# Kernel tuning notes

Measured on AMD Instinct MI355X. Metric: run time of the kernel, lower is better.

## Reference

```python
import jax, jax.numpy as jnp
import numpy as np

B, M, C, D, FF, FEAT = 1, 1024, 128, 512, 1024, 20
PAIR = 3 * D + 2 * FEAT  # slow_scorer_size = 1576


def _ffnn(x, W0, b0, W1, b1):
    # FFNN(depth=1): hidden relu layer then linear output (eval mode, no dropout)
    return jax.nn.relu(x @ W0 + b0) @ W1 + b1


def _batch_gather(x, idx):
    # x: [B, M, ...], idx: [B, ...] int -> gather along mention dim per batch
    return jax.vmap(lambda xb, ib: xb[ib])(x, idx)


def _bucket_distance(d):
    # log-scale distance buckets 0..9 (identity for d<=4)
    log_idx = jnp.floor(jnp.log(jnp.maximum(d, 1).astype(jnp.float32)) / jnp.log(2.0)).astype(jnp.int32) + 3
    return jnp.clip(jnp.where(d <= 4, d, log_idx), 0, 9)


def setup_inputs() -> dict:
    key = jax.random.key(0)
    ks = jax.random.split(key, 10)
    s = 0.02
    return {
        'mention_emb': jax.random.normal(ks[0], (B, M, D), dtype=jnp.float32),
        'mention_cluster_ids': jax.random.randint(ks[1], (B, M), 0, 200),
        'mention_speaker_ids': jax.random.randint(ks[2], (B, M), 0, 2),
        'ms_W0': jax.random.normal(ks[3], (D, FF), dtype=jnp.float32) * s,
        'ms_b0': jnp.zeros((FF,), jnp.float32),
        'ms_W1': jax.random.normal(ks[4], (FF, 1), dtype=jnp.float32) * s,
        'ms_b1': jnp.zeros((1,), jnp.float32),
        'sp_W0': jax.random.normal(ks[5], (PAIR, FF), dtype=jnp.float32) * s,
        'sp_b0': jnp.zeros((FF,), jnp.float32),
        'sp_W1': jax.random.normal(ks[6], (FF, 1), dtype=jnp.float32) * s,
        'sp_b1': jnp.zeros((1,), jnp.float32),
        'speaker_emb': jax.random.normal(ks[7], (2, FEAT), dtype=jnp.float32) * s,
        'bucket_emb': jax.random.normal(ks[8], (10, FEAT), dtype=jnp.float32) * s,
    }


def reference(mention_emb, mention_cluster_ids, mention_speaker_ids,
              ms_W0, ms_b0, ms_W1, ms_b1,
              sp_W0, sp_b0, sp_W1, sp_b1,
              speaker_emb, bucket_emb):
    # mention scoring
    mention_scores = _ffnn(mention_emb, ms_W0, ms_b0, ms_W1, ms_b1)[..., 0]  # [B, M]

    # get_antecedent_info: fixed window of C previous mentions
    offsets = jnp.arange(1, C + 1)[None, None, :]                    # [1,1,C]
    raw = jnp.arange(M)[None, :, None] - offsets                      # [1,M,C]
    antecedents = jnp.broadcast_to(jnp.clip(raw, 0, M - 1), (B, M, C))
    ant_mask = jnp.broadcast_to(raw >= 0, (B, M, C))

    fast_scores = _batch_gather(mention_scores, antecedents) + mention_scores[:, :, None]
    antecedent_emb = _batch_gather(mention_emb, antecedents)          # [B,M,C,D]

    # slow pair scorer features
    same_speaker = (_batch_gather(mention_speaker_ids, antecedents) == mention_speaker_ids[:, :, None]).astype(jnp.int32)
    speaker_feat = speaker_emb[same_speaker]                          # [B,M,C,FEAT]
    bucket_feat = jnp.broadcast_to(bucket_emb[_bucket_distance(offsets)], (B, M, C, FEAT))

    src = jnp.broadcast_to(mention_emb[:, :, None, :], (B, M, C, D))
    pair_emb = jnp.concatenate([src, antecedent_emb, src * antecedent_emb, speaker_feat, bucket_feat], axis=-1)
    slow_scores = _ffnn(pair_emb, sp_W0, sp_b0, sp_W1, sp_b1)[..., 0]  # [B,M,C]

    antecedent_scores = fast_scores + slow_scores + jnp.log(ant_mask.astype(jnp.float32))
    overall_scores = jnp.concatenate([jnp.zeros((B, M, 1), jnp.float32), antecedent_scores], axis=2)
    overall_dist = jax.nn.softmax(overall_scores, axis=-1)
    eps = 1e-6
    overall_dist = jnp.clip(overall_dist, eps, 1.0 - eps)
    overall_dist = overall_dist / jnp.sum(overall_dist, axis=-1, keepdims=True)

    # coref loss from cluster ids
    ant_cluster = _batch_gather(mention_cluster_ids, antecedents) * ant_mask.astype(mention_cluster_ids.dtype)
    same_cluster = ant_cluster == mention_cluster_ids[:, :, None]
    non_dummy = (mention_cluster_ids > 0)[:, :, None]
    ant_labels = same_cluster & non_dummy
    dummy_labels = ~jnp.any(ant_labels, axis=2, keepdims=True)
    overall_labels = jnp.concatenate([dummy_labels, ant_labels], axis=2)
    loss = -jnp.sum(jnp.log(overall_dist) * overall_labels.astype(jnp.float32), axis=2)
    loss = jnp.mean(jnp.sum(loss, axis=1))
    return overall_dist, loss
```

## Files before the change

### kernel.cpp

```cpp
#include <hip/hip_runtime.h>
#include <math.h>

#define MM 1024
#define DD 512
#define CC 128
#define LDSR 520


typedef __attribute__((ext_vector_type(8))) short bf16x8;
typedef __attribute__((ext_vector_type(4))) float f32x4;

__device__ __forceinline__ ushort bf16_rn(float x) {
    uint u = __float_as_uint(x);
    uint r = u + 0x7fffu + ((u >> 16) & 1u);
    return (ushort)(r >> 16);
}
__device__ __forceinline__ float bf16_to_f(ushort u) {
    return __uint_as_float(((uint)u) << 16);
}

__global__ __launch_bounds__(256) void prep_emb(const float* __restrict__ emb,
                                                ushort* __restrict__ embb)
{
    int i = blockIdx.x * 256 + threadIdx.x;
    float2 v = ((const float2*)emb)[i];
    ushort2 o;
    o.x = bf16_rn(v.x);
    o.y = bf16_rn(v.y);
    ((ushort2*)embb)[i] = o;
}

__global__ __launch_bounds__(256) void prep_wall(const float* __restrict__ ms_W0,
                                                 const float* __restrict__ sp_W0,
                                                 ushort* __restrict__ Wall)
{
    __shared__ float t[64][65];
    const int k0 = blockIdx.x * 64;
    const int n0 = blockIdx.y * 64;
    const int g = n0 >> 10;
    const float* src = (g == 0) ? ms_W0 : (sp_W0 + (size_t)(g - 1) * 512 * 1024);
    const int col0 = n0 & 1023;
    const int tr = threadIdx.x >> 6, tc = threadIdx.x & 63;
#pragma unroll
    for (int i = 0; i < 16; ++i) {
        int k = tr + i * 4;
        t[k][tc] = src[(size_t)(k0 + k) * 1024 + col0 + tc];
    }
    __syncthreads();
    const int f = threadIdx.x >> 2;
    const int c4 = threadIdx.x & 3;
    ushort tmp[16];
#pragma unroll
    for (int j = 0; j < 16; ++j) tmp[j] = bf16_rn(t[c4 * 16 + j][f]);
    uint4* dst = (uint4*)(Wall + (size_t)(n0 + f) * 512 + k0 + c4 * 16);
    dst[0] = *(uint4*)&tmp[0];
    dst[1] = *(uint4*)&tmp[8];
}

__global__ __launch_bounds__(256) void gemm_h_mfma(
    const ushort* __restrict__ embb, const ushort* __restrict__ Wall,
    float* __restrict__ H)
{
    const int n0 = blockIdx.x * 128;
    const int m0 = blockIdx.y * 128;
    const int lane = threadIdx.x & 63, wave = threadIdx.x >> 6;
    const int wx = wave & 1, wy = wave >> 1;
    const int l15 = lane & 15, lq = lane >> 4;

    const ushort* arow[4];
#pragma unroll
    for (int mi = 0; mi < 4; ++mi)
        arow[mi] = embb + (size_t)(m0 + wy * 64 + mi * 16 + l15) * 512;
    const ushort* brow[4];
#pragma unroll
    for (int ni = 0; ni < 4; ++ni)
        brow[ni] = Wall + (size_t)(n0 + wx * 64 + ni * 16 + l15) * 512;

    f32x4 acc[4][4];
#pragma unroll
    for (int i = 0; i < 4; ++i)
#pragma unroll
        for (int j = 0; j < 4; ++j) acc[i][j] = (f32x4)0.f;

    for (int kt = 0; kt < 512; kt += 32) {
        const int ko = kt + lq * 8;
        bf16x8 av[4], bv[4];
#pragma unroll
        for (int mi = 0; mi < 4; ++mi) av[mi] = *(const bf16x8*)(arow[mi] + ko);
#pragma unroll
        for (int ni = 0; ni < 4; ++ni) bv[ni] = *(const bf16x8*)(brow[ni] + ko);
#pragma unroll
        for (int mi = 0; mi < 4; ++mi)
#pragma unroll
            for (int ni = 0; ni < 4; ++ni)
                acc[mi][ni] = __builtin_amdgcn_mfma_f32_16x16x32_bf16(av[mi], bv[ni], acc[mi][ni], 0, 0, 0);
    }
#pragma unroll
    for (int mi = 0; mi < 4; ++mi)
#pragma unroll
        for (int r = 0; r < 4; ++r) {
            int mrow = m0 + wy * 64 + mi * 16 + lq * 4 + r;
#pragma unroll
            for (int ni = 0; ni < 4; ++ni)
                H[(size_t)mrow * 3072 + n0 + wx * 64 + ni * 16 + l15] = acc[mi][ni][r];
        }
}

__global__ void small_proj(const float* __restrict__ speaker_emb,
                           const float* __restrict__ bucket_emb,
                           const float* __restrict__ sp_W0,
                           float* __restrict__ spk_proj, float* __restrict__ bkt_proj)
{
    int r = blockIdx.x;
    const float* e; const float* W; float* out;
    if (r < 2) { e = speaker_emb + r * 20; W = sp_W0 + (size_t)1536 * 1024; out = spk_proj + r * 1024; }
    else       { e = bucket_emb + (r - 2) * 20; W = sp_W0 + (size_t)1556 * 1024; out = bkt_proj + (r - 2) * 1024; }
    float ek[20];
#pragma unroll
    for (int k = 0; k < 20; ++k) ek[k] = e[k];
    for (int f = threadIdx.x; f < 1024; f += blockDim.x) {
        float s = 0.f;
#pragma unroll
        for (int k = 0; k < 20; ++k) s = fmaf(ek[k], W[(size_t)k * 1024 + f], s);
        out[f] = s;
    }
}

__global__ __launch_bounds__(256) void mention_score(
    const float* __restrict__ H, const float* __restrict__ ms_b0,
    const float* __restrict__ ms_W1, const float* __restrict__ ms_b1,
    float* __restrict__ ms)
{
    int m = blockIdx.x;
    float v = 0.f;
    for (int f = threadIdx.x; f < 1024; f += 256) {
        float h = H[(size_t)m * 3072 + f] + ms_b0[f];
        v += fmaxf(h, 0.f) * ms_W1[f];
    }
#pragma unroll
    for (int o = 1; o < 64; o <<= 1) v += __shfl_xor(v, o);
    __shared__ float sm[4];
    if ((threadIdx.x & 63) == 0) sm[threadIdx.x >> 6] = v;
    __syncthreads();
    if (threadIdx.x == 0) ms[m] = sm[0] + sm[1] + sm[2] + sm[3] + ms_b1[0];
}

__global__ __launch_bounds__(512, 2) void pair_mfma(
    const ushort* __restrict__ embb, const ushort* __restrict__ Wt,
    const float* __restrict__ H, const float* __restrict__ spk_proj,
    const float* __restrict__ bkt_proj, const float* __restrict__ sp_b0,
    const float* __restrict__ sp_W1, const int* __restrict__ speaker,
    float* __restrict__ slow)
{
    extern __shared__ ushort Alds[];
    float* red = (float*)(Alds + 128 * LDSR);
    const int m = blockIdx.x;
    const int tid = threadIdx.x;

    {
        const int c = tid >> 2;
        const int kh = (tid & 3) * 128;
        int a = m - 1 - c; if (a < 0) a = 0;
        const ushort* ea = embb + (size_t)a * 512 + kh;
        const ushort* em = embb + (size_t)m * 512 + kh;
        ushort* dst = Alds + c * LDSR + kh;
        for (int j = 0; j < 128; j += 8) {
            bf16x8 va = *(const bf16x8*)(ea + j);
            bf16x8 vm = *(const bf16x8*)(em + j);
            uint pr[4];
#pragma unroll
            for (int p = 0; p < 4; ++p) {
                float q0 = bf16_to_f((ushort)va[2 * p])     * bf16_to_f((ushort)vm[2 * p]);
                float q1 = bf16_to_f((ushort)va[2 * p + 1]) * bf16_to_f((ushort)vm[2 * p + 1]);
                pr[p] = __builtin_amdgcn_perm(__float_as_uint(q1), __float_as_uint(q0), 0x07060302u);
            }
            *(bf16x8*)(dst + j) = *(bf16x8*)pr;
        }
    }
    __syncthreads();

    const int lane = tid & 63, wave = tid >> 6;
    const int l15 = lane & 15, lq = lane >> 4;
    const int spk_m = speaker[m];
    const ushort* aptr = Alds + l15 * LDSR + lq * 8;

    for (int pass = 0; pass < 2; ++pass) {
        const int cidx = pass * 8 + wave;
        const int f0 = cidx * 64;
        const ushort* brow[4];
#pragma unroll
        for (int ni = 0; ni < 4; ++ni) brow[ni] = Wt + (size_t)(f0 + ni * 16 + l15) * 512;

        f32x4 acc[8][4];
#pragma unroll
        for (int i = 0; i < 8; ++i)
#pragma unroll
            for (int j = 0; j < 4; ++j) acc[i][j] = (f32x4)0.f;

        bf16x8 a_c[8], b_c[4], a_n[8], b_n[4];
#pragma unroll
        for (int mi = 0; mi < 8; ++mi) a_c[mi] = *(const bf16x8*)(aptr + mi * 16 * LDSR);
#pragma unroll
        for (int ni = 0; ni < 4; ++ni) b_c[ni] = *(const bf16x8*)(brow[ni]);

        for (int kt = 0; kt < 512; kt += 32) {
            const int kn = (kt + 32) & 511;
#pragma unroll
            for (int mi = 0; mi < 8; ++mi) a_n[mi] = *(const bf16x8*)(aptr + mi * 16 * LDSR + kn);
#pragma unroll
            for (int ni = 0; ni < 4; ++ni) b_n[ni] = *(const bf16x8*)(brow[ni] + kn);
#pragma unroll
            for (int mi = 0; mi < 8; ++mi)
#pragma unroll
                for (int ni = 0; ni < 4; ++ni)
                    acc[mi][ni] = __builtin_amdgcn_mfma_f32_16x16x32_bf16(a_c[mi], b_c[ni], acc[mi][ni], 0, 0, 0);
#pragma unroll
            for (int mi = 0; mi < 8; ++mi) a_c[mi] = a_n[mi];
#pragma unroll
            for (int ni = 0; ni < 4; ++ni) b_c[ni] = b_n[ni];
        }

        float srcb[4], w1v[4], sp0[4], sp1[4], bk9[4];
#pragma unroll
        for (int ni = 0; ni < 4; ++ni) {
            int fcol = f0 + ni * 16 + l15;
            srcb[ni] = H[(size_t)m * 3072 + 1024 + fcol] + sp_b0[fcol];
            w1v[ni]  = sp_W1[fcol];
            sp0[ni]  = spk_proj[fcol];
            sp1[ni]  = spk_proj[1024 + fcol];
            bk9[ni]  = bkt_proj[9 * 1024 + fcol];
        }
#pragma unroll
        for (int mi = 0; mi < 8; ++mi) {
#pragma unroll
            for (int r = 0; r < 4; ++r) {
                const int c = mi * 16 + lq * 4 + r;
                int a = m - 1 - c; if (a < 0) a = 0;
                const int ss = (speaker[a] == spk_m) ? 1 : 0;
                const int off = c + 1;
                int bk;
                if (off <= 4) bk = off;
                else { bk = 31 - __clz(off) + 3; if (bk > 9) bk = 9; }
                const float* antp = H + (size_t)a * 3072 + 2048;
                float s = 0.f;
#pragma unroll
                for (int ni = 0; ni < 4; ++ni) {
                    const int fcol = f0 + ni * 16 + l15;
                    float bval = (mi >= 4) ? bk9[ni] : bkt_proj[(size_t)bk * 1024 + fcol];
                    float spv  = ss ? sp1[ni] : sp0[ni];
                    float pre = acc[mi][ni][r] + srcb[ni] + antp[fcol] + spv + bval;
                    s += fmaxf(pre, 0.f) * w1v[ni];
                }
                s += __shfl_xor(s, 1); s += __shfl_xor(s, 2);
                s += __shfl_xor(s, 4); s += __shfl_xor(s, 8);
                if (l15 == 0) red[cidx * 128 + c] = s;
            }
        }
    }
    __syncthreads();
    if (tid < 128) {
        float s = 0.f;
#pragma unroll
        for (int i = 0; i < 16; ++i) s += red[i * 128 + tid];
        slow[(size_t)m * 128 + tid] = s;
    }
}

__device__ __forceinline__ float bsum2(float v, float* sm) {
#pragma unroll
    for (int o = 1; o < 64; o <<= 1) v += __shfl_xor(v, o);
    __syncthreads();
    if ((threadIdx.x & 63) == 0) sm[threadIdx.x >> 6] = v;
    __syncthreads();
    return sm[0] + sm[1];
}
__device__ __forceinline__ float bmax2(float v, float* sm) {
#pragma unroll
    for (int o = 1; o < 64; o <<= 1) v = fmaxf(v, __shfl_xor(v, o));
    __syncthreads();
    if ((threadIdx.x & 63) == 0) sm[threadIdx.x >> 6] = v;
    __syncthreads();
    return fmaxf(sm[0], sm[1]);
}

__global__ __launch_bounds__(128) void softmax_loss(
    const float* __restrict__ slow, const float* __restrict__ ms,
    const float* __restrict__ sp_b1, const int* __restrict__ cluster,
    float* __restrict__ out, float* __restrict__ loss_partial)
{
    const int m = blockIdx.x, c = threadIdx.x;
    __shared__ float sm[2];
    const int raw = m - 1 - c;
    const bool maskv = raw >= 0;
    const int a = maskv ? raw : 0;
    float score = slow[(size_t)m * 128 + c] + sp_b1[0] + ms[m] + ms[a];
    if (!maskv) score = -INFINITY;

    float mx = fmaxf(bmax2(score, sm), 0.f);
    float e = expf(score - mx);
    float e0 = expf(0.f - mx);
    float sum = bsum2(e, sm) + e0;
    float p = e / sum, p0 = e0 / sum;
    const float eps = 1e-6f;
    p  = fminf(fmaxf(p,  eps), 1.f - eps);
    p0 = fminf(fmaxf(p0, eps), 1.f - eps);
    float sum2 = bsum2(p, sm) + p0;
    p /= sum2; p0 /= sum2;
    out[(size_t)m * 129 + 1 + c] = p;
    if (c == 0) out[(size_t)m * 129] = p0;

    const int cid = cluster[m];
    const bool lbl = maskv && (cid > 0) && (cluster[a] == cid);
    float anyc = bsum2(lbl ? 1.f : 0.f, sm);
    float lsum = bsum2(lbl ? -logf(p) : 0.f, sm);
    if (c == 0) {
        if (anyc == 0.f) lsum += -logf(p0);
        loss_partial[m] = lsum;
    }
}

__global__ void loss_sum(const float* __restrict__ lp, float* __restrict__ out) {
    float v = 0.f;
    for (int i = threadIdx.x; i < 1024; i += 256) v += lp[i];
#pragma unroll
    for (int o = 1; o < 64; o <<= 1) v += __shfl_xor(v, o);
    __shared__ float sm[4];
    if ((threadIdx.x & 63) == 0) sm[threadIdx.x >> 6] = v;
    __syncthreads();
    if (threadIdx.x == 0) out[(size_t)1024 * 129] = sm[0] + sm[1] + sm[2] + sm[3];
}

extern "C" void kernel_launch(void* const* d_in, const int* in_sizes, int n_in,
                              void* d_out, int out_size, void* d_ws, size_t ws_size,
                              hipStream_t stream)
{
    const float* emb   = (const float*)d_in[0];
    const int*   clus  = (const int*)  d_in[1];
    const int*   spk   = (const int*)  d_in[2];
    const float* ms_W0 = (const float*)d_in[3];
    const float* ms_b0 = (const float*)d_in[4];
    const float* ms_W1 = (const float*)d_in[5];
    const float* ms_b1 = (const float*)d_in[6];
    const float* sp_W0 = (const float*)d_in[7];
    const float* sp_b0 = (const float*)d_in[8];
    const float* sp_W1 = (const float*)d_in[9];
    const float* sp_b1 = (const float*)d_in[10];
    const float* spke  = (const float*)d_in[11];
    const float* bkte  = (const float*)d_in[12];

    float* ws = (float*)d_ws;
    float* H        = ws;
    float* slow     = ws + 3145728;
    float* spk_proj = ws + 3276800;
    float* bkt_proj = ws + 3278848;
    float* msc      = ws + 3289088;
    float* lossp    = ws + 3290112;
    ushort* embb    = (ushort*)(ws + 3291136);
    ushort* Wall    = (ushort*)(ws + 3553280);
    ushort* Wt      = Wall + (size_t)3072 * 512;
    float* out = (float*)d_out;

    static bool attr_set = false;
    if (!attr_set) {
        hipFuncSetAttribute((const void*)pair_mfma,
                            hipFuncAttributeMaxDynamicSharedMemorySize,
                            128 * LDSR * 2 + 16 * 128 * 4);
        attr_set = true;
    }

    hipLaunchKernelGGL(prep_emb, dim3(1024), dim3(256), 0, stream, emb, embb);
    hipLaunchKernelGGL(prep_wall, dim3(8, 64), dim3(256), 0, stream, ms_W0, sp_W0, Wall);
    hipLaunchKernelGGL(gemm_h_mfma, dim3(24, 8), dim3(256), 0, stream, embb, Wall, H);
    hipLaunchKernelGGL(small_proj, dim3(12), dim3(256), 0, stream, spke, bkte, sp_W0, spk_proj, bkt_proj);
    hipLaunchKernelGGL(mention_score, dim3(1024), dim3(256), 0, stream, H, ms_b0, ms_W1, ms_b1, msc);
    hipLaunchKernelGGL(pair_mfma, dim3(1024), dim3(512), 128 * LDSR * 2 + 16 * 128 * 4, stream,
                       embb, Wt, H, spk_proj, bkt_proj, sp_b0, sp_W1, spk, slow);
    hipLaunchKernelGGL(softmax_loss, dim3(1024), dim3(128), 0, stream,
                       slow, msc, sp_b1, clus, out, lossp);
    hipLaunchKernelGGL(loss_sum, dim3(1), dim3(256), 0, stream, lossp, out);
}
```

Measured before the change: 380.0 us.

## Rework pair kernel to 1024 threads with 32x32 MFMA tiles

The pair-scoring kernel now runs 16 waves per block, each owning one 64-column feature slice, instead of 8 waves doing two passes over slices. It switches from 16x16x32 to 32x32x16 bf16 MFMA, which takes fewer instructions and lower per-wave register load traffic. Speaker and bucket metadata are precomputed into LDS, and the LDS row stride is padded differently. The aim is more MFMA throughput and less redundant per-element index work, at the cost of larger blocks that reduce occupancy flexibility and a possible change in bank conflicts.

```diff
diff --git a/kernel.cpp b/kernel.cpp
--- a/kernel.cpp
+++ b/kernel.cpp
@@ -4,11 +4,12 @@
 #define MM 1024
 #define DD 512
 #define CC 128
-#define LDSR 520
+#define LDSR 528
 
 
 typedef __attribute__((ext_vector_type(8))) short bf16x8;
 typedef __attribute__((ext_vector_type(4))) float f32x4;
+typedef __attribute__((ext_vector_type(16))) float f32x16;
 
 __device__ __forceinline__ ushort bf16_rn(float x) {
     uint u = __float_as_uint(x);
@@ -145,7 +146,7 @@
     if (threadIdx.x == 0) ms[m] = sm[0] + sm[1] + sm[2] + sm[3] + ms_b1[0];
 }
 
-__global__ __launch_bounds__(512, 2) void pair_mfma(
+__global__ __launch_bounds__(1024) void pair_mfma(
     const ushort* __restrict__ embb, const ushort* __restrict__ Wt,
     const float* __restrict__ H, const float* __restrict__ spk_proj,
     const float* __restrict__ bkt_proj, const float* __restrict__ sp_b0,
@@ -154,17 +155,21 @@
 {
     extern __shared__ ushort Alds[];
     float* red = (float*)(Alds + 128 * LDSR);
+    int* meta_ss = (int*)(red + 16 * 128);
+    int* meta_bk = meta_ss + 128;
     const int m = blockIdx.x;
     const int tid = threadIdx.x;
+    const int spk_m = speaker[m];
 
     {
-        const int c = tid >> 2;
-        const int kh = (tid & 3) * 128;
+        const int c = tid >> 3;
+        const int kh = (tid & 7) * 64;
         int a = m - 1 - c; if (a < 0) a = 0;
         const ushort* ea = embb + (size_t)a * 512 + kh;
         const ushort* em = embb + (size_t)m * 512 + kh;
         ushort* dst = Alds + c * LDSR + kh;
-        for (int j = 0; j < 128; j += 8) {
+#pragma unroll
+        for (int j = 0; j < 64; j += 8) {
             bf16x8 va = *(const bf16x8*)(ea + j);
             bf16x8 vm = *(const bf16x8*)(em + j);
             uint pr[4];
@@ -176,84 +181,93 @@
             }
             *(bf16x8*)(dst + j) = *(bf16x8*)pr;
         }
-    }
-    __syncthreads();
-
-    const int lane = tid & 63, wave = tid >> 6;
-    const int l15 = lane & 15, lq = lane >> 4;
-    const int spk_m = speaker[m];
-    const ushort* aptr = Alds + l15 * LDSR + lq * 8;
+        if ((tid & 7) == 0) {
+            meta_ss[c] = (speaker[a] == spk_m) ? 1 : 0;
+            int off = c + 1;
+            int bk;
+            if (off <= 4) bk = off;
+            else { bk = 31 - __clz(off) + 3; if (bk > 9) bk = 9; }
+            meta_bk[c] = bk;
+        }
+    }
+    __syncthreads();
+
+    const int lane = tid & 63;
+    const int wave = __builtin_amdgcn_readfirstlane(tid >> 6);
+    const int l31 = lane & 31, k5 = lane >> 5;
+    const int f0 = wave * 64;
+
+    const ushort* bb0 = Wt + (size_t)f0 * 512 + l31 * 512 + k5 * 8;
+    const ushort* bb1 = bb0 + 32 * 512;
+    const ushort* abase = Alds + l31 * LDSR + k5 * 8;
+
+    float srcb[2], w1v[2], sp0v[2], sp1v[2], bk9v[2];
+#pragma unroll
+    for (int ni = 0; ni < 2; ++ni) {
+        int fcol = f0 + ni * 32 + l31;
+        srcb[ni] = H[(size_t)m * 3072 + 1024 + fcol] + sp_b0[fcol];
+        w1v[ni]  = sp_W1[fcol];
+        sp0v[ni] = spk_proj[fcol];
+        sp1v[ni] = spk_proj[1024 + fcol];
+        bk9v[ni] = bkt_proj[9 * 1024 + fcol];
+    }
 
     for (int pass = 0; pass < 2; ++pass) {
-        const int cidx = pass * 8 + wave;
-        const int f0 = cidx * 64;
-        const ushort* brow[4];
-#pragma unroll
-        for (int ni = 0; ni < 4; ++ni) brow[ni] = Wt + (size_t)(f0 + ni * 16 + l15) * 512;
-
-        f32x4 acc[8][4];
-#pragma unroll
-        for (int i = 0; i < 8; ++i)
-#pragma unroll
-            for (int j = 0; j < 4; ++j) acc[i][j] = (f32x4)0.f;
-
-        bf16x8 a_c[8], b_c[4], a_n[8], b_n[4];
-#pragma unroll
-        for (int mi = 0; mi < 8; ++mi) a_c[mi] = *(const bf16x8*)(aptr + mi * 16 * LDSR);
-#pragma unroll
-        for (int ni = 0; ni < 4; ++ni) b_c[ni] = *(const bf16x8*)(brow[ni]);
-
+        const int c0 = pass * 64;
+        const ushort* ap = abase + c0 * LDSR;
+        f32x16 acc[2][2];
+#pragma unroll
+        for (int i = 0; i < 2; ++i)
+#pragma unroll
+            for (int j = 0; j < 2; ++j) acc[i][j] = (f32x16)0.f;
+
+        bf16x8 aA[2], bA[2], aB[2], bB[2];
+        aA[0] = *(const bf16x8*)(ap);
+        aA[1] = *(const bf16x8*)(ap + 32 * LDSR);
+        bA[0] = *(const bf16x8*)(bb0);
+        bA[1] = *(const bf16x8*)(bb1);
         for (int kt = 0; kt < 512; kt += 32) {
-            const int kn = (kt + 32) & 511;
-#pragma unroll
-            for (int mi = 0; mi < 8; ++mi) a_n[mi] = *(const bf16x8*)(aptr + mi * 16 * LDSR + kn);
-#pragma unroll
-            for (int ni = 0; ni < 4; ++ni) b_n[ni] = *(const bf16x8*)(brow[ni] + kn);
-#pragma unroll
-            for (int mi = 0; mi < 8; ++mi)
-#pragma unroll
-                for (int ni = 0; ni < 4; ++ni)
-                    acc[mi][ni] = __builtin_amdgcn_mfma_f32_16x16x32_bf16(a_c[mi], b_c[ni], acc[mi][ni], 0, 0, 0);
-#pragma unroll
-            for (int mi = 0; mi < 8; ++mi) a_c[mi] = a_n[mi];
-#pragma unroll
-            for (int ni = 0; ni < 4; ++ni) b_c[ni] = b_n[ni];
-        }
-
-        float srcb[4], w1v[4], sp0[4], sp1[4], bk9[4];
-#pragma unroll
-        for (int ni = 0; ni < 4; ++ni) {
-            int fcol = f0 + ni * 16 + l15;
-            srcb[ni] = H[(size_t)m * 3072 + 1024 + fcol] + sp_b0[fcol];
-            w1v[ni]  = sp_W1[fcol];
-            sp0[ni]  = spk_proj[fcol];
-            sp1[ni]  = spk_proj[1024 + fcol];
-            bk9[ni]  = bkt_proj[9 * 1024 + fcol];
-        }
-#pragma unroll
-        for (int mi = 0; mi < 8; ++mi) {
-#pragma unroll
-            for (int r = 0; r < 4; ++r) {
-                const int c = mi * 16 + lq * 4 + r;
+            const int k1 = kt + 16;
+            aB[0] = *(const bf16x8*)(ap + k1);
+            aB[1] = *(const bf16x8*)(ap + 32 * LDSR + k1);
+            bB[0] = *(const bf16x8*)(bb0 + k1);
+            bB[1] = *(const bf16x8*)(bb1 + k1);
+#pragma unroll
+            for (int mi = 0; mi < 2; ++mi)
+#pragma unroll
+                for (int ni = 0; ni < 2; ++ni)
+                    acc[mi][ni] = __builtin_amdgcn_mfma_f32_32x32x16_bf16(aA[mi], bA[ni], acc[mi][ni], 0, 0, 0);
+            const int k2 = (kt + 32) & 511;
+            aA[0] = *(const bf16x8*)(ap + k2);
+            aA[1] = *(const bf16x8*)(ap + 32 * LDSR + k2);
+            bA[0] = *(const bf16x8*)(bb0 + k2);
+            bA[1] = *(const bf16x8*)(bb1 + k2);
+#pragma unroll
+            for (int mi = 0; mi < 2; ++mi)
+#pragma unroll
+                for (int ni = 0; ni < 2; ++ni)
+                    acc[mi][ni] = __builtin_amdgcn_mfma_f32_32x32x16_bf16(aB[mi], bB[ni], acc[mi][ni], 0, 0, 0);
+        }
+
+#pragma unroll
+        for (int mi = 0; mi < 2; ++mi) {
+#pragma unroll
+            for (int reg = 0; reg < 16; ++reg) {
+                const int c = c0 + mi * 32 + 4 * k5 + (reg & 3) + 8 * (reg >> 2);
                 int a = m - 1 - c; if (a < 0) a = 0;
-                const int ss = (speaker[a] == spk_m) ? 1 : 0;
-                const int off = c + 1;
-                int bk;
-                if (off <= 4) bk = off;
-                else { bk = 31 - __clz(off) + 3; if (bk > 9) bk = 9; }
+                const int ss = meta_ss[c];
                 const float* antp = H + (size_t)a * 3072 + 2048;
                 float s = 0.f;
 #pragma unroll
-                for (int ni = 0; ni < 4; ++ni) {
-                    const int fcol = f0 + ni * 16 + l15;
-                    float bval = (mi >= 4) ? bk9[ni] : bkt_proj[(size_t)bk * 1024 + fcol];
-                    float spv  = ss ? sp1[ni] : sp0[ni];
-                    float pre = acc[mi][ni][r] + srcb[ni] + antp[fcol] + spv + bval;
+                for (int ni = 0; ni < 2; ++ni) {
+                    const int fcol = f0 + ni * 32 + l31;
+                    float bval = pass ? bk9v[ni] : bkt_proj[(size_t)meta_bk[c] * 1024 + fcol];
+                    float pre = acc[mi][ni][reg] + srcb[ni] + antp[fcol] + (ss ? sp1v[ni] : sp0v[ni]) + bval;
                     s += fmaxf(pre, 0.f) * w1v[ni];
                 }
-                s += __shfl_xor(s, 1); s += __shfl_xor(s, 2);
-                s += __shfl_xor(s, 4); s += __shfl_xor(s, 8);
-                if (l15 == 0) red[cidx * 128 + c] = s;
+                s += __shfl_xor(s, 1); s += __shfl_xor(s, 2); s += __shfl_xor(s, 4);
+                s += __shfl_xor(s, 8); s += __shfl_xor(s, 16);
+                if (l31 == 0) red[wave * 128 + c] = s;
             }
         }
     }
@@ -360,11 +374,13 @@
     ushort* Wt      = Wall + (size_t)3072 * 512;
     float* out = (float*)d_out;
 
+    const int pair_lds = 128 * LDSR * 2 + 16 * 128 * 4 + 256 * 4;
+
     static bool attr_set = false;
     if (!attr_set) {
         hipFuncSetAttribute((const void*)pair_mfma,
                             hipFuncAttributeMaxDynamicSharedMemorySize,
-                            128 * LDSR * 2 + 16 * 128 * 4);
+                            pair_lds);
         attr_set = true;
     }
 
@@ -373,7 +389,7 @@
     hipLaunchKernelGGL(gemm_h_mfma, dim3(24, 8), dim3(256), 0, stream, embb, Wall, H);
     hipLaunchKernelGGL(small_proj, dim3(12), dim3(256), 0, stream, spke, bkte, sp_W0, spk_proj, bkt_proj);
     hipLaunchKernelGGL(mention_score, dim3(1024), dim3(256), 0, stream, H, ms_b0, ms_W1, ms_b1, msc);
-    hipLaunchKernelGGL(pair_mfma, dim3(1024), dim3(512), 128 * LDSR * 2 + 16 * 128 * 4, stream,
+    hipLaunchKernelGGL(pair_mfma, dim3(1024), dim3(1024), pair_lds, stream,
                        embb, Wt, H, spk_proj, bkt_proj, sp_b0, sp_W1, spk, slow);
     hipLaunchKernelGGL(softmax_loss, dim3(1024), dim3(128), 0, stream,
                        slow, msc, sp_b1, clus, out, lossp);
```

Measured after the change: 882.0 us. +132.1%, slower.
